# Performance work log

Hardware: AMD Instinct MI355X
Metric: run time of the kernel (lower is better)

Reference implementation:

```python
import jax, jax.numpy as jnp
import numpy as np

BOS, EOS, MAX_STEPS = 1, 2, 50
VOCAB, EMBD, HID, CTX, SEQ = 50257, 512, 1024, 1024, 50


def setup_inputs() -> dict:
    key = jax.random.key(0)
    ks = jax.random.split(key, 13)
    s = 0.05
    return {
        "seq_enc_states": jax.random.normal(ks[0], (SEQ, 1, CTX), jnp.float32),
        "seq_enc_hidden": jax.random.normal(ks[1], (1, CTX), jnp.float32),
        "E": jax.random.normal(ks[2], (VOCAB, EMBD), jnp.float32) * s,
        "W_init": jax.random.normal(ks[3], (HID, CTX), jnp.float32) * s,
        "b_init": jax.random.normal(ks[4], (HID,), jnp.float32) * s,
        "Wa": jax.random.normal(ks[5], (CTX, HID), jnp.float32) * s,
        "ba": jax.random.normal(ks[6], (CTX,), jnp.float32) * s,
        "W_ih": jax.random.normal(ks[7], (3 * HID, EMBD + CTX), jnp.float32) * s,
        "W_hh": jax.random.normal(ks[8], (3 * HID, HID), jnp.float32) * s,
        "b_ih": jax.random.normal(ks[9], (3 * HID,), jnp.float32) * s,
        "b_hh": jax.random.normal(ks[10], (3 * HID,), jnp.float32) * s,
        "Wv": jax.random.normal(ks[11], (VOCAB, HID), jnp.float32) * s,
        "bv": jax.random.normal(ks[12], (VOCAB,), jnp.float32) * s,
    }


def _gru_cell(x, h, W_ih, W_hh, b_ih, b_hh):
    # torch.nn.GRUCell math
    gi = x @ W_ih.T + b_ih  # (1, 3H)
    gh = h @ W_hh.T + b_hh  # (1, 3H)
    i_r, i_z, i_n = jnp.split(gi, 3, axis=-1)
    h_r, h_z, h_n = jnp.split(gh, 3, axis=-1)
    r = jax.nn.sigmoid(i_r + h_r)
    z = jax.nn.sigmoid(i_z + h_z)
    n = jnp.tanh(i_n + r * h_n)
    return (1.0 - z) * n + z * h


def reference(seq_enc_states, seq_enc_hidden, E, W_init, b_init, Wa, ba,
              W_ih, W_hh, b_ih, b_hh, Wv, bv):
    enc = seq_enc_states[:, 0, :]                       # (S, CTX)
    h0 = seq_enc_hidden.reshape(1, -1) @ W_init.T + b_init  # (1, H)
    emb0 = E[BOS][None, :]                              # (1, EMBD)

    def step(carry, _):
        h, emb, done = carry
        # dot-product attention over the 50 encoder positions
        ph = h @ Wa.T + ba                              # (1, CTX)
        attn = jax.nn.softmax(ph @ enc.T, axis=-1)      # (1, S)
        ctx = attn @ enc                                # (1, CTX)
        x = jnp.concatenate([emb, ctx], axis=-1)        # (1, EMBD+CTX)
        h_new = _gru_cell(x, h, W_ih, W_hh, b_ih, b_hh)
        logp = jax.nn.log_softmax(h_new @ Wv.T + bv, axis=-1)  # (1, V)
        idx = jnp.argmax(logp[0])
        valid = jnp.logical_not(done)
        is_eos = idx == EOS
        emit_idx = jnp.where(valid & jnp.logical_not(is_eos), idx, -1).astype(jnp.int32)
        logp_out = jnp.where(valid, logp[0], 0.0)
        new_emb = jnp.where((valid & jnp.logical_not(is_eos))[..., None], E[idx][None, :], emb)
        new_h = jnp.where(valid, h_new, h)
        new_done = done | is_eos
        return (new_h, new_emb, new_done), (emit_idx, logp_out, valid)

    init = (h0, emb0, jnp.array(False))
    _, (indices, logps, valid) = jax.lax.scan(step, init, None, length=MAX_STEPS)
    # indices: (50,) int32, -1 where past eos / eos itself (not appended in original)
    return indices, logps, valid
```

## Files before the change

kernel.cpp:

```cpp
#include <hip/hip_runtime.h>
#include <hip/hip_fp16.h>
#include <cmath>

#define VOCABSZ 50257
#define EMBD 512
#define HIDD 1024
#define CTXD 1024
#define SEQL 50
#define NSTEPS 50
#define BOS_ID 1
#define EOS_ID 2

#define NTHR 256
#define NB_GI 768
#define NB_WR 64
#define NB_PRE (NB_GI + NB_WR)
#define NB_LOG 832
#define NW_LOG (NB_LOG * 4)
#define NB_GHN 192

#define OFF_M      0
#define OFF_T      51200
#define OFF_H      51264
#define OFF_CTX    53312
#define OFF_GI     54336
#define OFF_GH     57408
#define OFF_L      60480
#define OFF_STATS  110784
#define OFF_STATE  117440
#define OFF_WVH    117568

__device__ __forceinline__ float wred_sum(float v) {
#pragma unroll
  for (int o = 32; o > 0; o >>= 1) v += __shfl_xor(v, o, 64);
  return v;
}

__device__ __forceinline__ float dot4(float4 a, float4 b) {
  return a.x * b.x + a.y * b.y + a.z * b.z + a.w * b.w;
}

__device__ __forceinline__ float wdot1024(const float* __restrict__ row, int lane,
                                          float4 b0, float4 b1, float4 b2, float4 b3) {
  const float4* r = (const float4*)row;
  float acc = dot4(r[lane], b0) + dot4(r[lane + 64], b1) +
              dot4(r[lane + 128], b2) + dot4(r[lane + 192], b3);
  return wred_sum(acc);
}

__device__ __forceinline__ bool beats(float v, int i, float v0, int i0) {
  return v > v0 || (v == v0 && i < i0);
}

__device__ __forceinline__ void top2_merge(float& v1, int& i1, float& v2, int& i2,
                                           float w1, int j1, float w2, int j2) {
  if (beats(w1, j1, v1, i1)) {
    float nv2; int ni2;
    if (beats(v1, i1, w2, j2)) { nv2 = v1; ni2 = i1; } else { nv2 = w2; ni2 = j2; }
    v1 = w1; i1 = j1; v2 = nv2; i2 = ni2;
  } else if (beats(w1, j1, v2, i2)) {
    v2 = w1; i2 = j1;
  }
}

__device__ __forceinline__ float acc8(uint4 a, const float* b) {
  const __half2* h = reinterpret_cast<const __half2*>(&a);
  float2 f0 = __half22float2(h[0]);
  float2 f1 = __half22float2(h[1]);
  float2 f2 = __half22float2(h[2]);
  float2 f3 = __half22float2(h[3]);
  return f0.x * b[0] + f0.y * b[1] + f1.x * b[2] + f1.y * b[3] +
         f2.x * b[4] + f2.y * b[5] + f3.x * b[6] + f3.y * b[7];
}

__global__ void __launch_bounds__(NTHR)
k_cvt(const float4* __restrict__ src, uint2* __restrict__ dst, int n4) {
  int i = blockIdx.x * NTHR + threadIdx.x;
  const int stride = gridDim.x * NTHR;
  for (; i < n4; i += stride) {
    float4 v = src[i];
    __half2 a = __floats2half2_rn(v.x, v.y);
    __half2 b = __floats2half2_rn(v.z, v.w);
    uint2 u;
    u.x = *reinterpret_cast<unsigned*>(&a);
    u.y = *reinterpret_cast<unsigned*>(&b);
    dst[i] = u;
  }
}

__global__ void __launch_bounds__(1024)
k0_matM(float* __restrict__ ws, const float* __restrict__ enc,
        const float* __restrict__ Wa) {
  const int kc = blockIdx.x;
  const int jg = blockIdx.y;
  const int tid = threadIdx.x;
  const int w = tid >> 6, lane = tid & 63;
  const int jw = w & 3, q = w >> 2;
  const int j = jg * 4 + jw;
  const int k = kc * 64 + lane;
  __shared__ float s_red[16][64];
  float acc0 = 0.f, acc1 = 0.f, acc2 = 0.f, acc3 = 0.f;
  if (j < SEQL) {
    const float4* e4 = (const float4*)(enc + (size_t)j * CTXD);
    const float* Wc = Wa + k;
    for (int c4 = q * 64; c4 < q * 64 + 64; ++c4) {
      float4 e = e4[c4];
      const float* wp = Wc + (size_t)(c4 * 4) * HIDD;
      acc0 += e.x * wp[0];
      acc1 += e.y * wp[HIDD];
      acc2 += e.z * wp[2 * HIDD];
      acc3 += e.w * wp[3 * HIDD];
    }
  }
  s_red[w][lane] = acc0 + acc1 + acc2 + acc3;
  __syncthreads();
  if (q == 0 && j < SEQL) {
    float v = s_red[jw][lane] + s_red[4 + jw][lane] +
              s_red[8 + jw][lane] + s_red[12 + jw][lane];
    ws[OFF_M + (size_t)j * HIDD + k] = v;
  }
}

__global__ void __launch_bounds__(NTHR)
k0_init(float* __restrict__ ws, const float* __restrict__ enc,
        const float* __restrict__ hid0, const float* __restrict__ Winit,
        const float* __restrict__ binit, const float* __restrict__ ba) {
  const int blk = blockIdx.x, tid = threadIdx.x;
  const int wave = tid >> 6, lane = tid & 63;
  if (blk == 0) {
    const float4* b4 = (const float4*)ba;
    float4 b0 = b4[lane], b1 = b4[lane + 64], b2 = b4[lane + 128], b3 = b4[lane + 192];
    for (int j = wave; j < SEQL; j += 4) {
      float v = wdot1024(enc + (size_t)j * CTXD, lane, b0, b1, b2, b3);
      if (lane == 0) ws[OFF_T + j] = v;
    }
    if (tid == 0) {
      int* st_emb = (int*)(ws + OFF_STATE);
      st_emb[0] = BOS_ID;
      st_emb[64] = 0;
    }
  } else {
    const float4* h4 = (const float4*)hid0;
    float4 b0 = h4[lane], b1 = h4[lane + 64], b2 = h4[lane + 128], b3 = h4[lane + 192];
    int row = (blk - 1) * 4 + wave;
    float v = wdot1024(Winit + (size_t)row * CTXD, lane, b0, b1, b2, b3) + binit[row];
    if (lane == 0) ws[OFF_H + row] = v;
  }
}

__device__ __forceinline__ void attn_from(float* __restrict__ ws, int hoff,
                                          const float* __restrict__ enc,
                                          int tid, int wave, int lane,
                                          float* s_h, float* s_sc, float* s_aw) {
  ((float4*)s_h)[tid] = ((const float4*)(ws + hoff))[tid];
  __syncthreads();
  const float4* h4 = (const float4*)s_h;
  float4 b0 = h4[lane], b1 = h4[lane + 64], b2 = h4[lane + 128], b3 = h4[lane + 192];
  for (int j = wave; j < SEQL; j += 4) {
    float v = wdot1024(ws + OFF_M + (size_t)j * HIDD, lane, b0, b1, b2, b3) + ws[OFF_T + j];
    if (lane == 0) s_sc[j] = v;
  }
  __syncthreads();
  if (tid < 64) {
    float v = (tid < SEQL) ? s_sc[tid] : -INFINITY;
    float mx = v;
#pragma unroll
    for (int o = 32; o > 0; o >>= 1) mx = fmaxf(mx, __shfl_xor(mx, o, 64));
    float e = (tid < SEQL) ? expf(v - mx) : 0.f;
    float sm = wred_sum(e);
    if (tid < SEQL) s_aw[tid] = e / sm;
  }
  __syncthreads();
  const float4* enc4 = (const float4*)enc;
  float4 acc = make_float4(0.f, 0.f, 0.f, 0.f);
  for (int j = 0; j < SEQL; ++j) {
    float a = s_aw[j];
    float4 ev = enc4[(size_t)j * (CTXD / 4) + tid];
    acc.x += a * ev.x; acc.y += a * ev.y; acc.z += a * ev.z; acc.w += a * ev.w;
  }
  ((float4*)(ws + OFF_CTX))[tid] = acc;
}

__global__ void __launch_bounds__(NTHR)
k_init2(float* __restrict__ ws, const float* __restrict__ enc,
        const float* __restrict__ Whh, const float* __restrict__ bhh) {
  const int blk = blockIdx.x, tid = threadIdx.x;
  const int wave = tid >> 6, lane = tid & 63;
  if (blk == 0) {
    __shared__ float s_h[HIDD];
    __shared__ float s_sc[64], s_aw[64];
    attn_from(ws, OFF_H, enc, tid, wave, lane, s_h, s_sc, s_aw);
  } else {
    const float4* h4 = (const float4*)(ws + OFF_H);
    float4 b0 = h4[lane], b1 = h4[lane + 64], b2 = h4[lane + 128], b3 = h4[lane + 192];
    const int r = (blk - 1) * 4 + wave;
    float v = wdot1024(Whh + (size_t)r * HIDD, lane, b0, b1, b2, b3) + bhh[r];
    if (lane == 0) ws[OFF_GH + r] = v;
  }
}

__global__ void __launch_bounds__(NTHR)
k_pre(float* __restrict__ ws, const float* __restrict__ E,
      const float* __restrict__ Wih, const float* __restrict__ bih,
      const float* __restrict__ Wv, const float* __restrict__ bv,
      float* __restrict__ out, int s) {
  const int blk = blockIdx.x, tid = threadIdx.x;
  const int wave = tid >> 6, lane = tid & 63;
  int* st_emb = (int*)(ws + OFF_STATE);
  int* st_done = st_emb + 64;
  const int hoff = OFF_H + (s & 1) * HIDD;

  const bool is_writer = (blk >= NB_GI);
  if (!is_writer && s >= NSTEPS) return;
  if (is_writer && s == 0) return;

  int emb_s = 0, D_s = 0, gidx = -1;
  float logZ = 0.f;
  bool valid = false, eos = false;

  if (s > 0) {
    __shared__ float rm[NTHR], rs_[NTHR], rv1[NTHR], rv2[NTHR];
    __shared__ int ri1[NTHR], ri2[NTHR];
    __shared__ float s_ex[2];
    float m = -INFINITY, su = 0.f, v1 = -INFINITY, v2 = -INFINITY;
    int i1 = 0x7fffffff, i2 = 0x7fffffff;
    const float4* sb = (const float4*)(ws + OFF_STATS);
    for (int q = tid; q < NB_LOG; q += NTHR) {
      float4 A = sb[q * 2];
      float4 B = sb[q * 2 + 1];
      float mn = fmaxf(m, A.x);
      su = ((m == -INFINITY) ? 0.f : su * __expf(m - mn)) + A.y * __expf(A.x - mn);
      m = mn;
      top2_merge(v1, i1, v2, i2, A.z, __float_as_int(A.w), B.x, __float_as_int(B.y));
    }
    rm[tid] = m; rs_[tid] = su; rv1[tid] = v1; ri1[tid] = i1; rv2[tid] = v2; ri2[tid] = i2;
    __syncthreads();
    for (int st = 128; st > 0; st >>= 1) {
      if (tid < st) {
        float m2 = rm[tid + st], s2 = rs_[tid + st];
        float mn = fmaxf(rm[tid], m2);
        rs_[tid] = rs_[tid] * __expf(rm[tid] - mn) + s2 * __expf(m2 - mn);
        rm[tid] = mn;
        float a1 = rv1[tid], a2 = rv2[tid];
        int b1 = ri1[tid], b2 = ri2[tid];
        top2_merge(a1, b1, a2, b2, rv1[tid + st], ri1[tid + st], rv2[tid + st], ri2[tid + st]);
        rv1[tid] = a1; ri1[tid] = b1; rv2[tid] = a2; ri2[tid] = b2;
      }
      __syncthreads();
    }
    const int fi1 = ri1[0], fi2 = ri2[0];
    if (wave < 2) {
      const float4* h4 = (const float4*)(ws + hoff);
      float4 b0 = h4[lane], b1 = h4[lane + 64], b2 = h4[lane + 128], b3 = h4[lane + 192];
      const int r = (wave == 0) ? fi1 : fi2;
      float v = wdot1024(Wv + (size_t)r * HIDD, lane, b0, b1, b2, b3) + bv[r];
      if (lane == 0) s_ex[wave] = v;
    }
    __syncthreads();
    gidx = beats(s_ex[1], fi2, s_ex[0], fi1) ? fi2 : fi1;
    logZ = rm[0] + logf(rs_[0]);
    const int Dp = st_done[s - 1];
    valid = (Dp == 0);
    eos = (gidx == EOS_ID);
    D_s = Dp | (eos ? 1 : 0);
    emb_s = (valid && !eos) ? gidx : st_emb[s - 1];
  } else {
    emb_s = st_emb[0];
  }

  if (!is_writer) {
    const int r = blk * 4 + wave;
    const float4* e4 = (const float4*)(E + (size_t)emb_s * EMBD);
    float4 eb0 = e4[lane], eb1 = e4[lane + 64];
    const float4* c4 = (const float4*)(ws + OFF_CTX);
    float4 cb0 = c4[lane], cb1 = c4[lane + 64], cb2 = c4[lane + 128], cb3 = c4[lane + 192];
    const float* rowp = Wih + (size_t)r * (EMBD + CTXD);
    const float4* re = (const float4*)rowp;
    const float4* rc = (const float4*)(rowp + EMBD);
    float acc = dot4(re[lane], eb0) + dot4(re[lane + 64], eb1) +
                dot4(rc[lane], cb0) + dot4(rc[lane + 64], cb1) +
                dot4(rc[lane + 128], cb2) + dot4(rc[lane + 192], cb3);
    float v = wred_sum(acc) + bih[r];
    if (lane == 0) ws[OFF_GI + r] = v;
  } else {
    if (blk == NB_GI && tid == 0) {
      out[s - 1] = (valid && !eos) ? (float)gidx : -1.f;
      out[NSTEPS + (size_t)NSTEPS * VOCABSZ + (s - 1)] = valid ? 1.f : 0.f;
      st_emb[s] = emb_s;
      st_done[s] = D_s;
    }
    float* logp = out + NSTEPS + (size_t)(s - 1) * VOCABSZ;
    for (int i = (blk - NB_GI) * NTHR + tid; i < VOCABSZ; i += NB_WR * NTHR)
      logp[i] = valid ? (ws[OFF_L + i] - logZ) : 0.f;
  }
}

__global__ void __launch_bounds__(NTHR)
k_logits(float* __restrict__ ws, const float* __restrict__ bv,
         const float* __restrict__ enc, const float* __restrict__ Whh,
         const float* __restrict__ bhh, int s) {
  const int blk = blockIdx.x, tid = threadIdx.x;
  const int wave = tid >> 6, lane = tid & 63;
  const int p = s & 1, np = p ^ 1;
  __shared__ float s_h[HIDD];

  const int* st_emb = (const int*)(ws + OFF_STATE);
  const int done = st_emb[64 + s];

  const float* hp = ws + OFF_H + p * HIDD;
#pragma unroll
  for (int it = 0; it < HIDD / NTHR; ++it) {
    const int i = tid + it * NTHR;
    float h = hp[i];
    if (done) {
      s_h[i] = h;
    } else {
      float r = 1.f / (1.f + __expf(-(ws[OFF_GI + i] + ws[OFF_GH + i])));
      float z = 1.f / (1.f + __expf(-(ws[OFF_GI + HIDD + i] + ws[OFF_GH + HIDD + i])));
      float n = tanhf(ws[OFF_GI + 2 * HIDD + i] + r * ws[OFF_GH + 2 * HIDD + i]);
      s_h[i] = (1.f - z) * n + z * h;
    }
  }
  __syncthreads();
  if (blk == 0) {
    ((float4*)(ws + OFF_H + np * HIDD))[tid] = ((const float4*)s_h)[tid];
  }

  if (blk > NB_LOG) {
    if (s + 1 >= NSTEPS) return;
    const float4* h4 = (const float4*)s_h;
    float4 b0 = h4[lane], b1 = h4[lane + 64], b2 = h4[lane + 128], b3 = h4[lane + 192];
    const int wid = (blk - NB_LOG - 1) * 4 + wave;
#pragma unroll
    for (int k = 0; k < 4; ++k) {
      const int r = wid + 768 * k;
      float v = wdot1024(Whh + (size_t)r * HIDD, lane, b0, b1, b2, b3) + bhh[r];
      if (lane == 0) ws[OFF_GH + r] = v;
    }
    return;
  }

  if (blk == NB_LOG) {
    if (s + 1 < NSTEPS) {
      __shared__ float s_sc[64], s_aw[64];
      const float4* h4 = (const float4*)s_h;
      float4 b0 = h4[lane], b1 = h4[lane + 64], b2 = h4[lane + 128], b3 = h4[lane + 192];
      for (int j = wave; j < SEQL; j += 4) {
        float v = wdot1024(ws + OFF_M + (size_t)j * HIDD, lane, b0, b1, b2, b3) + ws[OFF_T + j];
        if (lane == 0) s_sc[j] = v;
      }
      __syncthreads();
      if (tid < 64) {
        float v = (tid < SEQL) ? s_sc[tid] : -INFINITY;
        float mx = v;
#pragma unroll
        for (int o = 32; o > 0; o >>= 1) mx = fmaxf(mx, __shfl_xor(mx, o, 64));
        float e = (tid < SEQL) ? expf(v - mx) : 0.f;
        float smv = wred_sum(e);
        if (tid < SEQL) s_aw[tid] = e / smv;
      }
      __syncthreads();
      const float4* enc4 = (const float4*)enc;
      float4 acc = make_float4(0.f, 0.f, 0.f, 0.f);
      for (int j = 0; j < SEQL; ++j) {
        float a = s_aw[j];
        float4 ev = enc4[(size_t)j * (CTXD / 4) + tid];
        acc.x += a * ev.x; acc.y += a * ev.y; acc.z += a * ev.z; acc.w += a * ev.w;
      }
      ((float4*)(ws + OFF_CTX))[tid] = acc;
    }
    return;
  }

  __shared__ float sm[4], ssm[4], sv1[4], sv2[4];
  __shared__ int si1[4], si2[4];
  float hb[16];
  {
    const float4* h4 = (const float4*)s_h;
    float4 a = h4[lane * 2], b = h4[lane * 2 + 1];
    float4 c = h4[128 + lane * 2], d = h4[129 + lane * 2];
    hb[0] = a.x; hb[1] = a.y; hb[2] = a.z; hb[3] = a.w;
    hb[4] = b.x; hb[5] = b.y; hb[6] = b.z; hb[7] = b.w;
    hb[8] = c.x; hb[9] = c.y; hb[10] = c.z; hb[11] = c.w;
    hb[12] = d.x; hb[13] = d.y; hb[14] = d.z; hb[15] = d.w;
  }
  const __half* WvH = (const __half*)(ws + OFF_WVH);
  float m = -INFINITY, sum = 0.f, v1 = -INFINITY, v2 = -INFINITY;
  int i1 = 0x7fffffff, i2 = 0x7fffffff;
  for (int row = blk * 4 + wave; row < VOCABSZ; row += NW_LOG) {
    const uint4* r4 = (const uint4*)(WvH + (size_t)row * HIDD);
    float acc = acc8(r4[lane], hb) + acc8(r4[lane + 64], hb + 8);
    float l = wred_sum(acc) + bv[row];
    if (lane == 0) ws[OFF_L + row] = l;
    float mn = fmaxf(m, l);
    sum = ((m == -INFINITY) ? 0.f : sum * __expf(m - mn)) + __expf(l - mn);
    m = mn;
    if (beats(l, row, v1, i1)) { v2 = v1; i2 = i1; v1 = l; i1 = row; }
    else if (beats(l, row, v2, i2)) { v2 = l; i2 = row; }
  }
  if (lane == 0) {
    sm[wave] = m; ssm[wave] = sum;
    sv1[wave] = v1; si1[wave] = i1; sv2[wave] = v2; si2[wave] = i2;
  }
  __syncthreads();
  if (tid == 0) {
    float mm = sm[0], su = ssm[0], a1 = sv1[0], a2 = sv2[0];
    int b1 = si1[0], b2 = si2[0];
#pragma unroll
    for (int w = 1; w < 4; ++w) {
      float mn = fmaxf(mm, sm[w]);
      su = su * __expf(mm - mn) + ssm[w] * __expf(sm[w] - mn);
      mm = mn;
      top2_merge(a1, b1, a2, b2, sv1[w], si1[w], sv2[w], si2[w]);
    }
    float* st = ws + OFF_STATS + (size_t)blk * 8;
    st[0] = mm; st[1] = su;
    st[2] = a1; st[3] = __int_as_float(b1);
    st[4] = a2; st[5] = __int_as_float(b2);
  }
}

extern "C" void kernel_launch(void* const* d_in, const int* in_sizes, int n_in,
                              void* d_out, int out_size, void* d_ws, size_t ws_size,
                              hipStream_t stream) {
  const float* enc   = (const float*)d_in[0];
  const float* hid0  = (const float*)d_in[1];
  const float* E     = (const float*)d_in[2];
  const float* Winit = (const float*)d_in[3];
  const float* binit = (const float*)d_in[4];
  const float* Wa    = (const float*)d_in[5];
  const float* ba    = (const float*)d_in[6];
  const float* Wih   = (const float*)d_in[7];
  const float* Whh   = (const float*)d_in[8];
  const float* bih   = (const float*)d_in[9];
  const float* bhh   = (const float*)d_in[10];
  const float* Wv    = (const float*)d_in[11];
  const float* bv    = (const float*)d_in[12];
  float* out = (float*)d_out;
  float* ws  = (float*)d_ws;

  const int n4 = (VOCABSZ * HIDD) / 4;
  k_cvt<<<4096, NTHR, 0, stream>>>((const float4*)Wv, (uint2*)(ws + OFF_WVH), n4);
  k0_matM<<<dim3(16, 13), 1024, 0, stream>>>(ws, enc, Wa);
  k0_init<<<257, NTHR, 0, stream>>>(ws, enc, hid0, Winit, binit, ba);
  k_init2<<<769, NTHR, 0, stream>>>(ws, enc, Whh, bhh);
  for (int s = 0; s < NSTEPS; ++s) {
    k_pre<<<NB_PRE, NTHR, 0, stream>>>(ws, E, Wih, bih, Wv, bv, out, s);
    k_logits<<<NB_LOG + 1 + NB_GHN, NTHR, 0, stream>>>(ws, bv, enc, Whh, bhh, s);
  }
  k_pre<<<NB_PRE, NTHR, 0, stream>>>(ws, E, Wih, bih, Wv, bv, out, NSTEPS);
}
```

Measured before the change: 1.836 ms.

## Replace per-step kernel launches with a persistent cooperative kernel using grid syncs

The decode loop now runs inside one cooperative kernel of 512 blocks. Each step uses two grid-wide barriers instead of two kernel launches per step. Blocks are split into attention/context, W_hh gate, and fp16 vocab GEMV roles, and every block redundantly reduces the per-block softmax/top-2 stats to get the argmax. GH is double-buffered to avoid races, and launch overhead and inter-kernel gaps are the target. The risks are fewer blocks for the large vocab GEMV and grid-sync cost; a fallback to the old multi-launch path remains if the cooperative launch fails.

```diff
diff --git a/kernel.cpp b/kernel.cpp
--- a/kernel.cpp
+++ b/kernel.cpp
@@ -1,6 +1,9 @@
 #include <hip/hip_runtime.h>
+#include <hip/hip_cooperative_groups.h>
 #include <hip/hip_fp16.h>
 #include <cmath>
+
+namespace cg = cooperative_groups;
 
 #define VOCABSZ 50257
 #define EMBD 512
@@ -18,6 +21,15 @@
 #define NB_LOG 832
 #define NW_LOG (NB_LOG * 4)
 #define NB_GHN 192
+#define CNB 512
+#define C_GH_NB 56
+#define C_GEMV_B0 57
+#define C_NB_GEMV (CNB - C_GEMV_B0)
+#define C_NW_GEMV (C_NB_GEMV * 4)
+#define C_NW_GH (C_GH_NB * 4)
+#define C_WR_NB 64
+#define C_GI_B0 64
+#define C_NW_GI ((CNB - C_GI_B0) * 4)
 
 #define OFF_M      0
 #define OFF_T      51200
@@ -25,10 +37,10 @@
 #define OFF_CTX    53312
 #define OFF_GI     54336
 #define OFF_GH     57408
-#define OFF_L      60480
-#define OFF_STATS  110784
-#define OFF_STATE  117440
-#define OFF_WVH    117568
+#define OFF_L      63552
+#define OFF_STATS  113856
+#define OFF_STATE  120768
+#define OFF_WVH    120896
 
 __device__ __forceinline__ float wred_sum(float v) {
 #pragma unroll
@@ -308,6 +320,7 @@
   const int done = st_emb[64 + s];
 
   const float* hp = ws + OFF_H + p * HIDD;
+  const float* ghp = ws + OFF_GH + p * 3 * HIDD;
 #pragma unroll
   for (int it = 0; it < HIDD / NTHR; ++it) {
     const int i = tid + it * NTHR;
@@ -315,9 +328,9 @@
     if (done) {
       s_h[i] = h;
     } else {
-      float r = 1.f / (1.f + __expf(-(ws[OFF_GI + i] + ws[OFF_GH + i])));
-      float z = 1.f / (1.f + __expf(-(ws[OFF_GI + HIDD + i] + ws[OFF_GH + HIDD + i])));
-      float n = tanhf(ws[OFF_GI + 2 * HIDD + i] + r * ws[OFF_GH + 2 * HIDD + i]);
+      float r = 1.f / (1.f + __expf(-(ws[OFF_GI + i] + ghp[i])));
+      float z = 1.f / (1.f + __expf(-(ws[OFF_GI + HIDD + i] + ghp[HIDD + i])));
+      float n = tanhf(ws[OFF_GI + 2 * HIDD + i] + r * ghp[2 * HIDD + i]);
       s_h[i] = (1.f - z) * n + z * h;
     }
   }
@@ -335,7 +348,7 @@
     for (int k = 0; k < 4; ++k) {
       const int r = wid + 768 * k;
       float v = wdot1024(Whh + (size_t)r * HIDD, lane, b0, b1, b2, b3) + bhh[r];
-      if (lane == 0) ws[OFF_GH + r] = v;
+      if (lane == 0) ws[OFF_GH + np * 3 * HIDD + r] = v;
     }
     return;
   }
@@ -417,6 +430,207 @@
     st[0] = mm; st[1] = su;
     st[2] = a1; st[3] = __int_as_float(b1);
     st[4] = a2; st[5] = __int_as_float(b2);
+  }
+}
+
+__global__ void __launch_bounds__(NTHR, 2)
+k_coop(float* __restrict__ ws, const float* __restrict__ enc,
+       const float* __restrict__ E, const float* __restrict__ Wih,
+       const float* __restrict__ Whh, const float* __restrict__ bih,
+       const float* __restrict__ bhh, const float* __restrict__ Wv,
+       const float* __restrict__ bv, float* __restrict__ out) {
+  cg::grid_group grid = cg::this_grid();
+  const int blk = blockIdx.x, tid = threadIdx.x;
+  const int wave = tid >> 6, lane = tid & 63;
+  __shared__ float s_h[HIDD];
+  __shared__ float s_sc[64], s_aw[64];
+  __shared__ float rm[NTHR], rs_[NTHR], rv1[NTHR], rv2[NTHR];
+  __shared__ int ri1[NTHR], ri2[NTHR];
+  __shared__ float s_ex[2];
+
+  int emb = BOS_ID;
+  int done = 0;
+
+  ((float4*)s_h)[tid] = ((const float4*)(ws + OFF_H))[tid];
+  __syncthreads();
+
+  for (int s = 0; s < NSTEPS; ++s) {
+    const int p = s & 1, np = p ^ 1;
+
+    {
+      const float* ghp = ws + OFF_GH + p * 3 * HIDD;
+      if (!done) {
+#pragma unroll
+        for (int it = 0; it < HIDD / NTHR; ++it) {
+          const int i = tid + it * NTHR;
+          float h = s_h[i];
+          float r = 1.f / (1.f + __expf(-(ws[OFF_GI + i] + ghp[i])));
+          float z = 1.f / (1.f + __expf(-(ws[OFF_GI + HIDD + i] + ghp[HIDD + i])));
+          float n = tanhf(ws[OFF_GI + 2 * HIDD + i] + r * ghp[2 * HIDD + i]);
+          s_h[i] = (1.f - z) * n + z * h;
+        }
+      }
+      __syncthreads();
+    }
+
+    if (blk == 0) {
+      if (s + 1 < NSTEPS) {
+        const float4* h4 = (const float4*)s_h;
+        float4 b0 = h4[lane], b1 = h4[lane + 64], b2 = h4[lane + 128], b3 = h4[lane + 192];
+        for (int j = wave; j < SEQL; j += 4) {
+          float v = wdot1024(ws + OFF_M + (size_t)j * HIDD, lane, b0, b1, b2, b3) + ws[OFF_T + j];
+          if (lane == 0) s_sc[j] = v;
+        }
+        __syncthreads();
+        if (tid < 64) {
+          float v = (tid < SEQL) ? s_sc[tid] : -INFINITY;
+          float mx = v;
+#pragma unroll
+          for (int o = 32; o > 0; o >>= 1) mx = fmaxf(mx, __shfl_xor(mx, o, 64));
+          float e = (tid < SEQL) ? expf(v - mx) : 0.f;
+          float smv = wred_sum(e);
+          if (tid < SEQL) s_aw[tid] = e / smv;
+        }
+        __syncthreads();
+        const float4* enc4 = (const float4*)enc;
+        float4 acc = make_float4(0.f, 0.f, 0.f, 0.f);
+        for (int j = 0; j < SEQL; ++j) {
+          float a = s_aw[j];
+          float4 ev = enc4[(size_t)j * (CTXD / 4) + tid];
+          acc.x += a * ev.x; acc.y += a * ev.y; acc.z += a * ev.z; acc.w += a * ev.w;
+        }
+        ((float4*)(ws + OFF_CTX))[tid] = acc;
+      }
+    } else if (blk <= C_GH_NB) {
+      if (s + 1 < NSTEPS) {
+        const float4* h4 = (const float4*)s_h;
+        float4 b0 = h4[lane], b1 = h4[lane + 64], b2 = h4[lane + 128], b3 = h4[lane + 192];
+        const int wid = (blk - 1) * 4 + wave;
+        for (int r = wid; r < 3 * HIDD; r += C_NW_GH) {
+          float v = wdot1024(Whh + (size_t)r * HIDD, lane, b0, b1, b2, b3) + bhh[r];
+          if (lane == 0) ws[OFF_GH + np * 3 * HIDD + r] = v;
+        }
+      }
+    } else {
+      float hb[16];
+      {
+        const float4* h4 = (const float4*)s_h;
+        float4 a = h4[lane * 2], b = h4[lane * 2 + 1];
+        float4 c = h4[128 + lane * 2], d = h4[129 + lane * 2];
+        hb[0] = a.x; hb[1] = a.y; hb[2] = a.z; hb[3] = a.w;
+        hb[4] = b.x; hb[5] = b.y; hb[6] = b.z; hb[7] = b.w;
+        hb[8] = c.x; hb[9] = c.y; hb[10] = c.z; hb[11] = c.w;
+        hb[12] = d.x; hb[13] = d.y; hb[14] = d.z; hb[15] = d.w;
+      }
+      const __half* WvH = (const __half*)(ws + OFF_WVH);
+      float m = -INFINITY, sum = 0.f, v1 = -INFINITY, v2 = -INFINITY;
+      int i1 = 0x7fffffff, i2 = 0x7fffffff;
+      for (int row = (blk - C_GEMV_B0) * 4 + wave; row < VOCABSZ; row += C_NW_GEMV) {
+        const uint4* r4 = (const uint4*)(WvH + (size_t)row * HIDD);
+        float acc = acc8(r4[lane], hb) + acc8(r4[lane + 64], hb + 8);
+        float l = wred_sum(acc) + bv[row];
+        if (lane == 0) ws[OFF_L + row] = l;
+        float mn = fmaxf(m, l);
+        sum = ((m == -INFINITY) ? 0.f : sum * __expf(m - mn)) + __expf(l - mn);
+        m = mn;
+        if (beats(l, row, v1, i1)) { v2 = v1; i2 = i1; v1 = l; i1 = row; }
+        else if (beats(l, row, v2, i2)) { v2 = l; i2 = row; }
+      }
+      if (lane == 0) {
+        rm[wave] = m; rs_[wave] = sum;
+        rv1[wave] = v1; ri1[wave] = i1; rv2[wave] = v2; ri2[wave] = i2;
+      }
+      __syncthreads();
+      if (tid == 0) {
+        float mm = rm[0], su = rs_[0], a1 = rv1[0], a2 = rv2[0];
+        int b1 = ri1[0], b2 = ri2[0];
+#pragma unroll
+        for (int w = 1; w < 4; ++w) {
+          float mn = fmaxf(mm, rm[w]);
+          su = su * __expf(mm - mn) + rs_[w] * __expf(rm[w] - mn);
+          mm = mn;
+          top2_merge(a1, b1, a2, b2, rv1[w], ri1[w], rv2[w], ri2[w]);
+        }
+        float* st = ws + OFF_STATS + (size_t)(blk - C_GEMV_B0) * 8;
+        st[0] = mm; st[1] = su;
+        st[2] = a1; st[3] = __int_as_float(b1);
+        st[4] = a2; st[5] = __int_as_float(b2);
+      }
+    }
+    grid.sync();
+
+    {
+      float m = -INFINITY, su = 0.f, v1 = -INFINITY, v2 = -INFINITY;
+      int i1 = 0x7fffffff, i2 = 0x7fffffff;
+      const float4* sb = (const float4*)(ws + OFF_STATS);
+      for (int q = tid; q < C_NB_GEMV; q += NTHR) {
+        float4 A = sb[q * 2];
+        float4 B = sb[q * 2 + 1];
+        float mn = fmaxf(m, A.x);
+        su = ((m == -INFINITY) ? 0.f : su * __expf(m - mn)) + A.y * __expf(A.x - mn);
+        m = mn;
+        top2_merge(v1, i1, v2, i2, A.z, __float_as_int(A.w), B.x, __float_as_int(B.y));
+      }
+      rm[tid] = m; rs_[tid] = su; rv1[tid] = v1; ri1[tid] = i1; rv2[tid] = v2; ri2[tid] = i2;
+      __syncthreads();
+      for (int st = 128; st > 0; st >>= 1) {
+        if (tid < st) {
+          float m2 = rm[tid + st], s2 = rs_[tid + st];
+          float mn = fmaxf(rm[tid], m2);
+          rs_[tid] = rs_[tid] * __expf(rm[tid] - mn) + s2 * __expf(m2 - mn);
+          rm[tid] = mn;
+          float a1 = rv1[tid], a2 = rv2[tid];
+          int b1 = ri1[tid], b2 = ri2[tid];
+          top2_merge(a1, b1, a2, b2, rv1[tid + st], ri1[tid + st], rv2[tid + st], ri2[tid + st]);
+          rv1[tid] = a1; ri1[tid] = b1; rv2[tid] = a2; ri2[tid] = b2;
+        }
+        __syncthreads();
+      }
+      const int fi1 = ri1[0], fi2 = ri2[0];
+      if (wave < 2) {
+        const float4* h4 = (const float4*)s_h;
+        float4 b0 = h4[lane], b1 = h4[lane + 64], b2 = h4[lane + 128], b3 = h4[lane + 192];
+        const int r = (wave == 0) ? fi1 : fi2;
+        float v = wdot1024(Wv + (size_t)r * HIDD, lane, b0, b1, b2, b3) + bv[r];
+        if (lane == 0) s_ex[wave] = v;
+      }
+      __syncthreads();
+      const int gidx = beats(s_ex[1], fi2, s_ex[0], fi1) ? fi2 : fi1;
+      const float logZ = rm[0] + logf(rs_[0]);
+      const bool valid = (done == 0);
+      const bool eos = (gidx == EOS_ID);
+      __syncthreads();
+
+      if (blk == 0 && tid == 0) {
+        out[s] = (valid && !eos) ? (float)gidx : -1.f;
+        out[NSTEPS + (size_t)NSTEPS * VOCABSZ + s] = valid ? 1.f : 0.f;
+      }
+      if (blk < C_WR_NB) {
+        float* logp = out + NSTEPS + (size_t)s * VOCABSZ;
+        for (int i = blk * NTHR + tid; i < VOCABSZ; i += C_WR_NB * NTHR)
+          logp[i] = valid ? (ws[OFF_L + i] - logZ) : 0.f;
+      } else if (s + 1 < NSTEPS) {
+        const int emb_n = (valid && !eos) ? gidx : emb;
+        const int wid = (blk - C_GI_B0) * 4 + wave;
+        for (int r = wid; r < 3 * HIDD; r += C_NW_GI) {
+          const float4* e4 = (const float4*)(E + (size_t)emb_n * EMBD);
+          float4 eb0 = e4[lane], eb1 = e4[lane + 64];
+          const float4* c4 = (const float4*)(ws + OFF_CTX);
+          float4 cb0 = c4[lane], cb1 = c4[lane + 64], cb2 = c4[lane + 128], cb3 = c4[lane + 192];
+          const float* rowp = Wih + (size_t)r * (EMBD + CTXD);
+          const float4* re = (const float4*)rowp;
+          const float4* rc = (const float4*)(rowp + EMBD);
+          float acc = dot4(re[lane], eb0) + dot4(re[lane + 64], eb1) +
+                      dot4(rc[lane], cb0) + dot4(rc[lane + 64], cb1) +
+                      dot4(rc[lane + 128], cb2) + dot4(rc[lane + 192], cb3);
+          float v = wred_sum(acc) + bih[r];
+          if (lane == 0) ws[OFF_GI + r] = v;
+        }
+      }
+      emb = (valid && !eos) ? gidx : emb;
+      done = done | (eos ? 1 : 0);
+    }
+    grid.sync();
   }
 }
 
@@ -444,9 +658,19 @@
   k0_matM<<<dim3(16, 13), 1024, 0, stream>>>(ws, enc, Wa);
   k0_init<<<257, NTHR, 0, stream>>>(ws, enc, hid0, Winit, binit, ba);
   k_init2<<<769, NTHR, 0, stream>>>(ws, enc, Whh, bhh);
-  for (int s = 0; s < NSTEPS; ++s) {
-    k_pre<<<NB_PRE, NTHR, 0, stream>>>(ws, E, Wih, bih, Wv, bv, out, s);
-    k_logits<<<NB_LOG + 1 + NB_GHN, NTHR, 0, stream>>>(ws, bv, enc, Whh, bhh, s);
-  }
-  k_pre<<<NB_PRE, NTHR, 0, stream>>>(ws, E, Wih, bih, Wv, bv, out, NSTEPS);
-}
+  k_pre<<<NB_PRE, NTHR, 0, stream>>>(ws, E, Wih, bih, Wv, bv, out, 0);
+
+  void* cargs[10] = {(void*)&ws, (void*)&enc, (void*)&E, (void*)&Wih,
+                     (void*)&Whh, (void*)&bih, (void*)&bhh, (void*)&Wv,
+                     (void*)&bv, (void*)&out};
+  hipError_t ce = hipLaunchCooperativeKernel((void*)k_coop, dim3(CNB), dim3(NTHR),
+                                             cargs, 0, stream);
+  if (ce != hipSuccess) {
+    (void)hipGetLastError();
+    for (int s = 0; s < NSTEPS; ++s) {
+      if (s > 0) k_pre<<<NB_PRE, NTHR, 0, stream>>>(ws, E, Wih, bih, Wv, bv, out, s);
+      k_logits<<<NB_LOG + 1 + NB_GHN, NTHR, 0, stream>>>(ws, bv, enc, Whh, bhh, s);
+    }
+    k_pre<<<NB_PRE, NTHR, 0, stream>>>(ws, E, Wih, bih, Wv, bv, out, NSTEPS);
+  }
+}
```

Result: slower. 6.876 ms (+274.5%).

## Move log-prob writeback into next logits kernel and skip work after EOS

Applied to the files above, without the earlier changes.

Double-buffers the logits and GH workspace so the log-softmax output write for step s-1 can be done by extra blocks in the following k_logits launch, overlapping it with the next step's GEMV work instead of serialising it in k_pre. A dedicated state block in k_pre publishes logZ and the valid flag for those writer blocks. It also adds early exits after the sequence is done, skipping the GI, GH, attention and logits computation. The workspace layout grows, and correctness relies on the parity indexing of the new buffers being consistent.

```diff
diff --git a/kernel.cpp b/kernel.cpp
--- a/kernel.cpp
+++ b/kernel.cpp
@@ -14,10 +14,17 @@
 #define NTHR 256
 #define NB_GI 768
 #define NB_WR 64
-#define NB_PRE (NB_GI + NB_WR)
 #define NB_LOG 832
 #define NW_LOG (NB_LOG * 4)
 #define NB_GHN 192
+#define KL_ATTN NB_LOG
+#define KL_GH0 (NB_LOG + 1)
+#define KL_WR0 (NB_LOG + 1 + NB_GHN)
+#define KL_GRID (KL_WR0 + NB_WR)
+#define PRE_GRID (NB_GI + 1)
+#define PRE_GRID_FIN (NB_GI + 1 + NB_WR)
+
+#define LPAD 50304
 
 #define OFF_M      0
 #define OFF_T      51200
@@ -25,10 +32,10 @@
 #define OFF_CTX    53312
 #define OFF_GI     54336
 #define OFF_GH     57408
-#define OFF_L      60480
-#define OFF_STATS  110784
-#define OFF_STATE  117440
-#define OFF_WVH    117568
+#define OFF_L      63552
+#define OFF_STATS  164160
+#define OFF_STATE  170816
+#define OFF_WVH    171072
 
 __device__ __forceinline__ float wred_sum(float v) {
 #pragma unroll
@@ -210,9 +217,11 @@
   int* st_done = st_emb + 64;
   const int hoff = OFF_H + (s & 1) * HIDD;
 
-  const bool is_writer = (blk >= NB_GI);
-  if (!is_writer && s >= NSTEPS) return;
-  if (is_writer && s == 0) return;
+  const bool is_gi = (blk < NB_GI);
+  const bool is_state = (blk == NB_GI);
+  const bool is_writer = (blk > NB_GI);
+  if (is_gi && s >= NSTEPS) return;
+  if ((is_state || is_writer) && s == 0) return;
 
   int emb_s = 0, D_s = 0, gidx = -1;
   float logZ = 0.f;
@@ -268,7 +277,8 @@
     emb_s = st_emb[0];
   }
 
-  if (!is_writer) {
+  if (is_gi) {
+    if (D_s) return;
     const int r = blk * 4 + wave;
     const float4* e4 = (const float4*)(E + (size_t)emb_s * EMBD);
     float4 eb0 = e4[lane], eb1 = e4[lane + 64];
@@ -282,32 +292,48 @@
                 dot4(rc[lane + 128], cb2) + dot4(rc[lane + 192], cb3);
     float v = wred_sum(acc) + bih[r];
     if (lane == 0) ws[OFF_GI + r] = v;
-  } else {
-    if (blk == NB_GI && tid == 0) {
+  } else if (is_state) {
+    if (tid == 0) {
       out[s - 1] = (valid && !eos) ? (float)gidx : -1.f;
       out[NSTEPS + (size_t)NSTEPS * VOCABSZ + (s - 1)] = valid ? 1.f : 0.f;
       st_emb[s] = emb_s;
       st_done[s] = D_s;
-    }
+      ws[OFF_STATE + 128] = logZ;
+      ws[OFF_STATE + 129] = valid ? 1.f : 0.f;
+    }
+  } else {
+    const float* Lp = ws + OFF_L + (size_t)((s - 1) & 1) * LPAD;
     float* logp = out + NSTEPS + (size_t)(s - 1) * VOCABSZ;
-    for (int i = (blk - NB_GI) * NTHR + tid; i < VOCABSZ; i += NB_WR * NTHR)
-      logp[i] = valid ? (ws[OFF_L + i] - logZ) : 0.f;
+    for (int i = (blk - NB_GI - 1) * NTHR + tid; i < VOCABSZ; i += NB_WR * NTHR)
+      logp[i] = valid ? (Lp[i] - logZ) : 0.f;
   }
 }
 
 __global__ void __launch_bounds__(NTHR)
 k_logits(float* __restrict__ ws, const float* __restrict__ bv,
          const float* __restrict__ enc, const float* __restrict__ Whh,
-         const float* __restrict__ bhh, int s) {
+         const float* __restrict__ bhh, float* __restrict__ out, int s) {
   const int blk = blockIdx.x, tid = threadIdx.x;
   const int wave = tid >> 6, lane = tid & 63;
   const int p = s & 1, np = p ^ 1;
+
+  if (blk >= KL_WR0) {
+    if (s == 0) return;
+    const float logZ = ws[OFF_STATE + 128];
+    const bool valid = ws[OFF_STATE + 129] != 0.f;
+    const float* Lp = ws + OFF_L + (size_t)np * LPAD;
+    float* logp = out + NSTEPS + (size_t)(s - 1) * VOCABSZ;
+    for (int i = (blk - KL_WR0) * NTHR + tid; i < VOCABSZ; i += NB_WR * NTHR)
+      logp[i] = valid ? (Lp[i] - logZ) : 0.f;
+    return;
+  }
+
   __shared__ float s_h[HIDD];
-
   const int* st_emb = (const int*)(ws + OFF_STATE);
   const int done = st_emb[64 + s];
 
   const float* hp = ws + OFF_H + p * HIDD;
+  const float* ghp = ws + OFF_GH + p * 3 * HIDD;
 #pragma unroll
   for (int it = 0; it < HIDD / NTHR; ++it) {
     const int i = tid + it * NTHR;
@@ -315,9 +341,9 @@
     if (done) {
       s_h[i] = h;
     } else {
-      float r = 1.f / (1.f + __expf(-(ws[OFF_GI + i] + ws[OFF_GH + i])));
-      float z = 1.f / (1.f + __expf(-(ws[OFF_GI + HIDD + i] + ws[OFF_GH + HIDD + i])));
-      float n = tanhf(ws[OFF_GI + 2 * HIDD + i] + r * ws[OFF_GH + 2 * HIDD + i]);
+      float r = 1.f / (1.f + __expf(-(ws[OFF_GI + i] + ghp[i])));
+      float z = 1.f / (1.f + __expf(-(ws[OFF_GI + HIDD + i] + ghp[HIDD + i])));
+      float n = tanhf(ws[OFF_GI + 2 * HIDD + i] + r * ghp[2 * HIDD + i]);
       s_h[i] = (1.f - z) * n + z * h;
     }
   }
@@ -326,52 +352,52 @@
     ((float4*)(ws + OFF_H + np * HIDD))[tid] = ((const float4*)s_h)[tid];
   }
 
-  if (blk > NB_LOG) {
-    if (s + 1 >= NSTEPS) return;
+  if (blk >= KL_GH0) {
+    if (s + 1 >= NSTEPS || done) return;
     const float4* h4 = (const float4*)s_h;
     float4 b0 = h4[lane], b1 = h4[lane + 64], b2 = h4[lane + 128], b3 = h4[lane + 192];
-    const int wid = (blk - NB_LOG - 1) * 4 + wave;
+    const int wid = (blk - KL_GH0) * 4 + wave;
 #pragma unroll
     for (int k = 0; k < 4; ++k) {
       const int r = wid + 768 * k;
       float v = wdot1024(Whh + (size_t)r * HIDD, lane, b0, b1, b2, b3) + bhh[r];
-      if (lane == 0) ws[OFF_GH + r] = v;
+      if (lane == 0) ws[OFF_GH + np * 3 * HIDD + r] = v;
     }
     return;
   }
 
-  if (blk == NB_LOG) {
-    if (s + 1 < NSTEPS) {
-      __shared__ float s_sc[64], s_aw[64];
-      const float4* h4 = (const float4*)s_h;
-      float4 b0 = h4[lane], b1 = h4[lane + 64], b2 = h4[lane + 128], b3 = h4[lane + 192];
-      for (int j = wave; j < SEQL; j += 4) {
-        float v = wdot1024(ws + OFF_M + (size_t)j * HIDD, lane, b0, b1, b2, b3) + ws[OFF_T + j];
-        if (lane == 0) s_sc[j] = v;
-      }
-      __syncthreads();
-      if (tid < 64) {
-        float v = (tid < SEQL) ? s_sc[tid] : -INFINITY;
-        float mx = v;
-#pragma unroll
-        for (int o = 32; o > 0; o >>= 1) mx = fmaxf(mx, __shfl_xor(mx, o, 64));
-        float e = (tid < SEQL) ? expf(v - mx) : 0.f;
-        float smv = wred_sum(e);
-        if (tid < SEQL) s_aw[tid] = e / smv;
-      }
-      __syncthreads();
-      const float4* enc4 = (const float4*)enc;
-      float4 acc = make_float4(0.f, 0.f, 0.f, 0.f);
-      for (int j = 0; j < SEQL; ++j) {
-        float a = s_aw[j];
-        float4 ev = enc4[(size_t)j * (CTXD / 4) + tid];
-        acc.x += a * ev.x; acc.y += a * ev.y; acc.z += a * ev.z; acc.w += a * ev.w;
-      }
-      ((float4*)(ws + OFF_CTX))[tid] = acc;
-    }
+  if (blk == KL_ATTN) {
+    if (s + 1 >= NSTEPS || done) return;
+    __shared__ float s_sc[64], s_aw[64];
+    const float4* h4 = (const float4*)s_h;
+    float4 b0 = h4[lane], b1 = h4[lane + 64], b2 = h4[lane + 128], b3 = h4[lane + 192];
+    for (int j = wave; j < SEQL; j += 4) {
+      float v = wdot1024(ws + OFF_M + (size_t)j * HIDD, lane, b0, b1, b2, b3) + ws[OFF_T + j];
+      if (lane == 0) s_sc[j] = v;
+    }
+    __syncthreads();
+    if (tid < 64) {
+      float v = (tid < SEQL) ? s_sc[tid] : -INFINITY;
+      float mx = v;
+#pragma unroll
+      for (int o = 32; o > 0; o >>= 1) mx = fmaxf(mx, __shfl_xor(mx, o, 64));
+      float e = (tid < SEQL) ? expf(v - mx) : 0.f;
+      float smv = wred_sum(e);
+      if (tid < SEQL) s_aw[tid] = e / smv;
+    }
+    __syncthreads();
+    const float4* enc4 = (const float4*)enc;
+    float4 acc = make_float4(0.f, 0.f, 0.f, 0.f);
+    for (int j = 0; j < SEQL; ++j) {
+      float a = s_aw[j];
+      float4 ev = enc4[(size_t)j * (CTXD / 4) + tid];
+      acc.x += a * ev.x; acc.y += a * ev.y; acc.z += a * ev.z; acc.w += a * ev.w;
+    }
+    ((float4*)(ws + OFF_CTX))[tid] = acc;
     return;
   }
 
+  if (done) return;
   __shared__ float sm[4], ssm[4], sv1[4], sv2[4];
   __shared__ int si1[4], si2[4];
   float hb[16];
@@ -385,13 +411,14 @@
     hb[12] = d.x; hb[13] = d.y; hb[14] = d.z; hb[15] = d.w;
   }
   const __half* WvH = (const __half*)(ws + OFF_WVH);
+  float* Lc = ws + OFF_L + (size_t)p * LPAD;
   float m = -INFINITY, sum = 0.f, v1 = -INFINITY, v2 = -INFINITY;
   int i1 = 0x7fffffff, i2 = 0x7fffffff;
   for (int row = blk * 4 + wave; row < VOCABSZ; row += NW_LOG) {
     const uint4* r4 = (const uint4*)(WvH + (size_t)row * HIDD);
     float acc = acc8(r4[lane], hb) + acc8(r4[lane + 64], hb + 8);
     float l = wred_sum(acc) + bv[row];
-    if (lane == 0) ws[OFF_L + row] = l;
+    if (lane == 0) Lc[row] = l;
     float mn = fmaxf(m, l);
     sum = ((m == -INFINITY) ? 0.f : sum * __expf(m - mn)) + __expf(l - mn);
     m = mn;
@@ -445,8 +472,8 @@
   k0_init<<<257, NTHR, 0, stream>>>(ws, enc, hid0, Winit, binit, ba);
   k_init2<<<769, NTHR, 0, stream>>>(ws, enc, Whh, bhh);
   for (int s = 0; s < NSTEPS; ++s) {
-    k_pre<<<NB_PRE, NTHR, 0, stream>>>(ws, E, Wih, bih, Wv, bv, out, s);
-    k_logits<<<NB_LOG + 1 + NB_GHN, NTHR, 0, stream>>>(ws, bv, enc, Whh, bhh, s);
-  }
-  k_pre<<<NB_PRE, NTHR, 0, stream>>>(ws, E, Wih, bih, Wv, bv, out, NSTEPS);
-}
+    k_pre<<<PRE_GRID, NTHR, 0, stream>>>(ws, E, Wih, bih, Wv, bv, out, s);
+    k_logits<<<KL_GRID, NTHR, 0, stream>>>(ws, bv, enc, Whh, bhh, out, s);
+  }
+  k_pre<<<PRE_GRID_FIN, NTHR, 0, stream>>>(ws, E, Wih, bih, Wv, bv, out, NSTEPS);
+}
```

Result: no change. 1.826 ms, median of 2 (-0.6%).
